# Kernel tuning notes

Hardware: AMD Instinct MI355X
Metric: run time of the kernel (lower is better)

The kernel has to match this reference:

```python
import jax, jax.numpy as jnp
import numpy as np

B, N, D_IN, D_OUT = 16, 2048, 128, 128

def setup_inputs() -> dict:
    key = jax.random.key(0)
    ks = jax.random.split(key, 8)
    x = jax.random.normal(ks[0], (B, N, D_IN), dtype=jnp.float32)
    adj = jax.random.randint(ks[1], (N, N), 0, 2).astype(jnp.float32)
    # Conv1d(kernel_size=1) weights, PyTorch default uniform init scale
    s_emb = 1.0 / np.sqrt(D_IN)
    W_emb = jax.random.uniform(ks[2], (D_OUT, D_IN), jnp.float32, -s_emb, s_emb)
    b_emb = jax.random.uniform(ks[3], (D_OUT,), jnp.float32, -s_emb, s_emb)
    s_qk = 1.0 / np.sqrt(D_OUT)
    w_q = jax.random.uniform(ks[4], (D_OUT,), jnp.float32, -s_qk, s_qk)
    b_q = jax.random.uniform(ks[5], (1,), jnp.float32, -s_qk, s_qk)
    w_k = jax.random.uniform(ks[6], (D_OUT,), jnp.float32, -s_qk, s_qk)
    b_k = jax.random.uniform(ks[7], (1,), jnp.float32, -s_qk, s_qk)
    return {"x": x, "adj": adj, "W_emb": W_emb, "b_emb": b_emb,
            "w_q": w_q, "b_q": b_q, "w_k": w_k, "b_k": b_k}

def reference(x, adj, W_emb, b_emb, w_q, b_q, w_k, b_k):
    # emb_conv: 1x1 conv over node dim == per-node linear  [B,N,D_out]
    seq_fts = jnp.einsum('bni,oi->bno', x, W_emb) + b_emb
    # q_conv / k_conv: project to scalar per node  [B,N]
    q = jnp.einsum('bnd,d->bn', seq_fts, w_q) + b_q  # f_1_t squeezed
    k = jnp.einsum('bnd,d->bn', seq_fts, w_k) + b_k  # f_2_t squeezed
    # f[b,i,j] = f_1_t[b,0,j] + f_2_t^T[b,i,0] = q[b,j] + k[b,i]
    f = k[:, :, None] + q[:, None, :]                 # [B,N,N]
    f = jax.nn.leaky_relu(adj[None, :, :] * f, negative_slope=0.01)
    coefs = jax.nn.softmax(f, axis=1)                 # softmax over dim=1 (rows)
    vals = jnp.einsum('bij,bjd->bid', coefs, seq_fts)  # [B,N,D_out]
    return vals
```

## Files before the change

kernel.cpp:

```cpp
#include <hip/hip_runtime.h>
#include <hip/hip_bf16.h>
#include <stdint.h>

#define B_ 16
#define N_ 2048
#define D_ 128

typedef __bf16 bf16_t;
typedef bf16_t bf16x8 __attribute__((ext_vector_type(8)));
typedef float f32x4 __attribute__((ext_vector_type(4)));

__global__ __launch_bounds__(256) void k_pack_adj(const float* __restrict__ adj,
                                                  unsigned int* __restrict__ bits) {
    int t = blockIdx.x * 256 + threadIdx.x;
    float v = adj[t];
    unsigned long long m = __ballot(v > 0.5f);
    if ((t & 63) == 0) {
        int i = t >> 11;
        int j = t & 2047;
        bits[i * 64 + (j >> 5)]     = (unsigned int)m;
        bits[i * 64 + (j >> 5) + 1] = (unsigned int)(m >> 32);
    }
}

__global__ __launch_bounds__(256, 2) void k_emb(const float* __restrict__ x,
                                                const float* __restrict__ W,
                                                const float* __restrict__ be,
                                                const float* __restrict__ wq,
                                                const float* __restrict__ bq,
                                                const float* __restrict__ wk,
                                                const float* __restrict__ bk,
                                                float* __restrict__ sfT,
                                                float* __restrict__ qa, float* __restrict__ ka,
                                                float* __restrict__ Eq, float* __restrict__ eqs,
                                                float* __restrict__ Ek, float* __restrict__ eks) {
    __shared__ float xs[32][68];
    __shared__ float ws[32][132];
    __shared__ float qs[64], ks[64];
    int b  = blockIdx.y;
    int n0 = blockIdx.x * 64;
    int tid = threadIdx.x;
    int tx = tid & 15, ty = tid >> 4;
    if (tid < 64) { qs[tid] = 0.f; ks[tid] = 0.f; }

    float acc[4][8] = {};
    f32x4 xr[2], wr[4];

    auto loadregs = [&](int kc) {
#pragma unroll
        for (int s = 0; s < 2; ++s) {
            int p = tid + 256 * s;
            int n = p >> 3, kq = p & 7;
            xr[s] = *(const f32x4*)(x + ((size_t)(b * N_ + n0 + n)) * D_ + kc * 32 + kq * 4);
        }
#pragma unroll
        for (int s = 0; s < 4; ++s) {
            int p = tid + 256 * s;
            int d = p >> 3, kq = p & 7;
            wr[s] = *(const f32x4*)(W + (size_t)d * D_ + kc * 32 + kq * 4);
        }
    };
    auto writelds = [&]() {
#pragma unroll
        for (int s = 0; s < 2; ++s) {
            int p = tid + 256 * s;
            int n = p >> 3, kq = p & 7;
#pragma unroll
            for (int u = 0; u < 4; ++u) xs[kq * 4 + u][n] = xr[s][u];
        }
#pragma unroll
        for (int s = 0; s < 4; ++s) {
            int p = tid + 256 * s;
            int d = p >> 3, kq = p & 7;
#pragma unroll
            for (int u = 0; u < 4; ++u) ws[kq * 4 + u][d] = wr[s][u];
        }
    };

    loadregs(0);
    for (int kc = 0; kc < 4; ++kc) {
        writelds();
        __syncthreads();
        if (kc < 3) loadregs(kc + 1);
#pragma unroll 4
        for (int k = 0; k < 32; ++k) {
            f32x4 xv  = *(const f32x4*)&xs[k][tx * 4];
            f32x4 wv0 = *(const f32x4*)&ws[k][ty * 8];
            f32x4 wv1 = *(const f32x4*)&ws[k][ty * 8 + 4];
#pragma unroll
            for (int i = 0; i < 4; ++i)
#pragma unroll
                for (int j = 0; j < 8; ++j)
                    acc[i][j] += xv[i] * ((j < 4) ? wv0[j] : wv1[j - 4]);
        }
        __syncthreads();
    }

    float qp[4] = {}, kp[4] = {};
#pragma unroll
    for (int j = 0; j < 8; ++j) {
        int d = ty * 8 + j;
        float bj  = be[d];
        float wqj = wq[d];
        float wkj = wk[d];
        f32x4 o;
#pragma unroll
        for (int i = 0; i < 4; ++i) {
            o[i] = acc[i][j] + bj;
            qp[i] += o[i] * wqj;
            kp[i] += o[i] * wkj;
        }
        *(f32x4*)(sfT + ((size_t)b * D_ + d) * N_ + n0 + tx * 4) = o;
    }
#pragma unroll
    for (int i = 0; i < 4; ++i) {
        atomicAdd(&qs[tx * 4 + i], qp[i]);
        atomicAdd(&ks[tx * 4 + i], kp[i]);
    }
    __syncthreads();
    if (tid < 64) {
        int idx = b * N_ + n0 + tid;
        float aq = qs[tid] + bq[0];
        float ak = ks[tid] + bk[0];
        qa[idx] = aq;          ka[idx] = ak;
        Eq[idx] = expf(aq);    eqs[idx] = expf(0.01f * aq);
        Ek[idx] = expf(ak);    eks[idx] = expf(0.01f * ak);
    }
}

__global__ __launch_bounds__(256) void k_denom(const unsigned int* __restrict__ bits,
                                               const float* __restrict__ qa,
                                               const float* __restrict__ ka,
                                               const float* __restrict__ Eq,
                                               const float* __restrict__ eqs,
                                               const float* __restrict__ Ek,
                                               const float* __restrict__ eks,
                                               float* __restrict__ denom) {
    int jt  = blockIdx.x;
    int b   = blockIdx.y;
    int seg = blockIdx.z;
    int j = jt * 256 + threadIdx.x;
    float qj  = qa[b * N_ + j];
    float Eqj = Eq[b * N_ + j];
    float eqj = eqs[b * N_ + j];
    int shift = j & 31;
    int wid   = j >> 5;
    float acc = 0.f;
    int i0 = seg * 256;
#pragma unroll 16
    for (int i = i0; i < i0 + 256; ++i) {
        float kk  = ka[b * N_ + i];
        float Ekk = Ek[b * N_ + i];
        float ekk = eks[b * N_ + i];
        unsigned int w = bits[i * 64 + wid];
        float z  = kk + qj;
        float f1 = z > 0.f ? Ekk : ekk;
        float f2 = z > 0.f ? Eqj : eqj;
        float v  = f1 * f2;
        acc += ((w >> shift) & 1u) ? v : 1.0f;
    }
    atomicAdd(&denom[b * N_ + j], acc);
}

__global__ __launch_bounds__(256) void k_scale(const float* __restrict__ sfT,
                                               const float* __restrict__ denom,
                                               bf16_t* __restrict__ Pt) {
    size_t t4 = ((size_t)blockIdx.x * 256 + threadIdx.x) * 4;
    int j  = (int)(t4 & (N_ - 1));
    int b  = (int)(t4 >> 18);
    f32x4 sv = *(const f32x4*)(sfT + t4);
    f32x4 dv = *(const f32x4*)(denom + b * N_ + j);
    bf16_t o[4];
#pragma unroll
    for (int u = 0; u < 4; ++u)
        o[u] = (bf16_t)(sv[u] * __builtin_amdgcn_rcpf(dv[u]));
    *(uint2*)(Pt + t4) = *(uint2*)o;
}

__global__ __launch_bounds__(512, 2) void k_attn(const float* __restrict__ qa,
                                                 const float* __restrict__ ka,
                                                 const float* __restrict__ Eq,
                                                 const float* __restrict__ eqs,
                                                 const float* __restrict__ Ek,
                                                 const float* __restrict__ eks,
                                                 const unsigned int* __restrict__ bits,
                                                 const bf16_t* __restrict__ Pt,
                                                 float* __restrict__ out) {
    __shared__ __align__(16) bf16_t lds[2][128 * 64];
    int b     = blockIdx.y;
    int ibase = blockIdx.x * 128;
    int tid   = threadIdx.x;
    int w     = tid >> 6;
    int lane  = tid & 63;
    int m16   = lane & 15;
    int quad  = lane >> 4;
    int ig    = w & 3;
    int d0    = (w >> 2) * 64;
    int i0    = ibase + ig * 32;

    int iA = i0 + m16, iB = i0 + 16 + m16;
    float kR0  = ka[b * N_ + iA],  kR1  = ka[b * N_ + iB];
    float EkR0 = Ek[b * N_ + iA],  EkR1 = Ek[b * N_ + iB];
    float ekR0 = eks[b * N_ + iA], ekR1 = eks[b * N_ + iB];
    const unsigned int* br0 = bits + (size_t)iA * 64;
    const unsigned int* br1 = bits + (size_t)iB * 64;
    const float* qp  = qa  + b * N_;
    const float* Eqp = Eq  + b * N_;
    const float* eqp = eqs + b * N_;
    const bf16_t* PtB = Pt + (size_t)b * D_ * N_;

    f32x4 acc[2][4];
#pragma unroll
    for (int c = 0; c < 2; ++c)
#pragma unroll
        for (int nt = 0; nt < 4; ++nt) acc[c][nt] = (f32x4){0.f, 0.f, 0.f, 0.f};

    auto stage = [&](int bufi, int jb) {
#pragma unroll
        for (int t = 0; t < 2; ++t) {
            int off = (w * 2 + t) * 1024 + lane * 16;
            int d   = off >> 7;
            int g   = ((off & 127) >> 4) ^ (d & 7);
            const bf16_t* gp = PtB + (size_t)d * N_ + jb + g * 8;
            __builtin_amdgcn_global_load_lds(
                (const __attribute__((address_space(1))) void*)gp,
                (__attribute__((address_space(3))) void*)((char*)(&lds[bufi][0]) + (w * 2 + t) * 1024),
                16, 0, 0);
        }
    };

    stage(0, 0);
    __syncthreads();
    int buf = 0;
    for (int step = 0; step < N_ / 64; ++step) {
        int jb = step * 64;
        if (step + 1 < N_ / 64) stage(buf ^ 1, jb + 64);

        f32x4 q0[2], q1[2], E0[2], E1[2], e0[2], e1[2];
#pragma unroll
        for (int h = 0; h < 2; ++h) {
            int j0 = jb + h * 32 + quad * 8;
            q0[h] = *(const f32x4*)(qp  + j0);
            q1[h] = *(const f32x4*)(qp  + j0 + 4);
            E0[h] = *(const f32x4*)(Eqp + j0);
            E1[h] = *(const f32x4*)(Eqp + j0 + 4);
            e0[h] = *(const f32x4*)(eqp + j0);
            e1[h] = *(const f32x4*)(eqp + j0 + 4);
        }
        uint2 wb0 = *(const uint2*)&br0[jb >> 5];
        uint2 wb1 = *(const uint2*)&br1[jb >> 5];

        bf16x8 af[2][2];
#pragma unroll
        for (int h = 0; h < 2; ++h) {
            unsigned int w0 = h ? wb0.y : wb0.x;
            unsigned int w1 = h ? wb1.y : wb1.x;
#pragma unroll
            for (int t = 0; t < 8; ++t) {
                float qv = (t < 4) ? q0[h][t] : q1[h][t - 4];
                float Ev = (t < 4) ? E0[h][t] : E1[h][t - 4];
                float ev = (t < 4) ? e0[h][t] : e1[h][t - 4];
                int bit = quad * 8 + t;
                {
                    float z = kR0 + qv;
                    float v = ((z > 0.f) ? EkR0 : ekR0) * ((z > 0.f) ? Ev : ev);
                    af[0][h][t] = (bf16_t)(((w0 >> bit) & 1u) ? v : 1.0f);
                }
                {
                    float z = kR1 + qv;
                    float v = ((z > 0.f) ? EkR1 : ekR1) * ((z > 0.f) ? Ev : ev);
                    af[1][h][t] = (bf16_t)(((w1 >> bit) & 1u) ? v : 1.0f);
                }
            }
        }

#pragma unroll
        for (int h = 0; h < 2; ++h) {
            int cph = ((h * 4 + quad) ^ (m16 & 7)) * 8;
#pragma unroll
            for (int nt = 0; nt < 4; ++nt) {
                int d = d0 + nt * 16 + m16;
                bf16x8 bf = *(const bf16x8*)&lds[buf][d * 64 + cph];
                acc[0][nt] = __builtin_amdgcn_mfma_f32_16x16x32_bf16(af[0][h], bf, acc[0][nt], 0, 0, 0);
                acc[1][nt] = __builtin_amdgcn_mfma_f32_16x16x32_bf16(af[1][h], bf, acc[1][nt], 0, 0, 0);
            }
        }
        __syncthreads();
        buf ^= 1;
    }

#pragma unroll
    for (int c = 0; c < 2; ++c) {
        int irow = i0 + c * 16 + quad * 4;
#pragma unroll
        for (int nt = 0; nt < 4; ++nt) {
            int d = d0 + nt * 16 + m16;
#pragma unroll
            for (int r = 0; r < 4; ++r)
                out[((size_t)b * N_ + irow + r) * D_ + d] = acc[c][nt][r];
        }
    }
}

extern "C" void kernel_launch(void* const* d_in, const int* in_sizes, int n_in,
                              void* d_out, int out_size, void* d_ws, size_t ws_size,
                              hipStream_t stream) {
    const float* x   = (const float*)d_in[0];
    const float* adj = (const float*)d_in[1];
    const float* W   = (const float*)d_in[2];
    const float* be  = (const float*)d_in[3];
    const float* wq  = (const float*)d_in[4];
    const float* bq  = (const float*)d_in[5];
    const float* wk  = (const float*)d_in[6];
    const float* bk  = (const float*)d_in[7];
    float* out = (float*)d_out;

    char* ws = (char*)d_ws;
    size_t off = 0;
    float* sfT = (float*)(ws + off);  off += (size_t)B_ * D_ * N_ * 4;
    bf16_t* Pt = (bf16_t*)(ws + off); off += (size_t)B_ * D_ * N_ * 2;
    float* qa  = (float*)(ws + off);  off += (size_t)B_ * N_ * 4;
    float* ka  = (float*)(ws + off);  off += (size_t)B_ * N_ * 4;
    float* denom = (float*)(ws + off); off += (size_t)B_ * N_ * 4;
    float* Eq  = (float*)(ws + off);  off += (size_t)B_ * N_ * 4;
    float* eqs = (float*)(ws + off);  off += (size_t)B_ * N_ * 4;
    float* Ek  = (float*)(ws + off);  off += (size_t)B_ * N_ * 4;
    float* eks = (float*)(ws + off);  off += (size_t)B_ * N_ * 4;
    unsigned int* bits = (unsigned int*)(ws + off); off += (size_t)N_ * 64 * 4;

    hipMemsetAsync(denom, 0, (size_t)B_ * N_ * 4, stream);

    k_pack_adj<<<N_ * N_ / 256, 256, 0, stream>>>(adj, bits);
    k_emb<<<dim3(N_ / 64, B_), 256, 0, stream>>>(x, W, be, wq, bq, wk, bk,
                                                 sfT, qa, ka, Eq, eqs, Ek, eks);
    k_denom<<<dim3(8, 16, 8), 256, 0, stream>>>(bits, qa, ka, Eq, eqs, Ek, eks, denom);
    k_scale<<<B_ * D_ * N_ / 1024, 256, 0, stream>>>(sfT, denom, Pt);
    k_attn<<<dim3(N_ / 128, B_), 512, 0, stream>>>(qa, ka, Eq, eqs, Ek, eks, bits, Pt, out);
}
```

Before: 216.1 us.

## Share computed attention A-fragments across waves via LDS in k_attn

Measured after the change: 204.3 us. -5.5%, faster.

```diff
diff --git a/kernel.cpp b/kernel.cpp
--- a/kernel.cpp
+++ b/kernel.cpp
@@ -177,7 +177,7 @@
     *(uint2*)(Pt + t4) = *(uint2*)o;
 }
 
-__global__ __launch_bounds__(512, 2) void k_attn(const float* __restrict__ qa,
+__global__ __launch_bounds__(256, 2) void k_attn(const float* __restrict__ qa,
                                                  const float* __restrict__ ka,
                                                  const float* __restrict__ Eq,
                                                  const float* __restrict__ eqs,
@@ -186,24 +186,26 @@
                                                  const unsigned int* __restrict__ bits,
                                                  const bf16_t* __restrict__ Pt,
                                                  float* __restrict__ out) {
-    __shared__ __align__(16) bf16_t lds[2][128 * 64];
+    __shared__ __align__(16) bf16_t ldsB[2][128 * 64];
+    __shared__ __align__(16) bf16_t ldsA[4 * 2 * 64 * 8];
     int b     = blockIdx.y;
-    int ibase = blockIdx.x * 128;
+    int ibase = blockIdx.x * 64;
     int tid   = threadIdx.x;
     int w     = tid >> 6;
     int lane  = tid & 63;
     int m16   = lane & 15;
     int quad  = lane >> 4;
-    int ig    = w & 3;
-    int d0    = (w >> 2) * 64;
-    int i0    = ibase + ig * 32;
-
-    int iA = i0 + m16, iB = i0 + 16 + m16;
+    int ig    = w & 1;
+    int dg    = w >> 1;
+    int h     = dg;
+
+    int iA = ibase + (2 * ig) * 16 + m16;
+    int iB = iA + 16;
     float kR0  = ka[b * N_ + iA],  kR1  = ka[b * N_ + iB];
     float EkR0 = Ek[b * N_ + iA],  EkR1 = Ek[b * N_ + iB];
     float ekR0 = eks[b * N_ + iA], ekR1 = eks[b * N_ + iB];
-    const unsigned int* br0 = bits + (size_t)iA * 64;
-    const unsigned int* br1 = bits + (size_t)iB * 64;
+    const unsigned int* brA = bits + (size_t)iA * 64;
+    const unsigned int* brB = bits + (size_t)iB * 64;
     const float* qp  = qa  + b * N_;
     const float* Eqp = Eq  + b * N_;
     const float* eqp = eqs + b * N_;
@@ -217,14 +219,14 @@
 
     auto stage = [&](int bufi, int jb) {
 #pragma unroll
-        for (int t = 0; t < 2; ++t) {
-            int off = (w * 2 + t) * 1024 + lane * 16;
+        for (int t = 0; t < 4; ++t) {
+            int off = t * 4096 + tid * 16;
             int d   = off >> 7;
             int g   = ((off & 127) >> 4) ^ (d & 7);
             const bf16_t* gp = PtB + (size_t)d * N_ + jb + g * 8;
             __builtin_amdgcn_global_load_lds(
                 (const __attribute__((address_space(1))) void*)gp,
-                (__attribute__((address_space(3))) void*)((char*)(&lds[bufi][0]) + (w * 2 + t) * 1024),
+                (__attribute__((address_space(3))) void*)((char*)(&ldsB[bufi][0]) + off),
                 16, 0, 0);
         }
     };
@@ -234,55 +236,54 @@
     int buf = 0;
     for (int step = 0; step < N_ / 64; ++step) {
         int jb = step * 64;
+
+        int j0 = jb + h * 32 + quad * 8;
+        f32x4 q0 = *(const f32x4*)(qp  + j0);
+        f32x4 q1 = *(const f32x4*)(qp  + j0 + 4);
+        f32x4 E0 = *(const f32x4*)(Eqp + j0);
+        f32x4 E1 = *(const f32x4*)(Eqp + j0 + 4);
+        f32x4 e0 = *(const f32x4*)(eqp + j0);
+        f32x4 e1 = *(const f32x4*)(eqp + j0 + 4);
+        unsigned int wA = brA[(jb >> 5) + h];
+        unsigned int wB = brB[(jb >> 5) + h];
+        __builtin_amdgcn_sched_barrier(0);
+
         if (step + 1 < N_ / 64) stage(buf ^ 1, jb + 64);
 
-        f32x4 q0[2], q1[2], E0[2], E1[2], e0[2], e1[2];
-#pragma unroll
-        for (int h = 0; h < 2; ++h) {
-            int j0 = jb + h * 32 + quad * 8;
-            q0[h] = *(const f32x4*)(qp  + j0);
-            q1[h] = *(const f32x4*)(qp  + j0 + 4);
-            E0[h] = *(const f32x4*)(Eqp + j0);
-            E1[h] = *(const f32x4*)(Eqp + j0 + 4);
-            e0[h] = *(const f32x4*)(eqp + j0);
-            e1[h] = *(const f32x4*)(eqp + j0 + 4);
-        }
-        uint2 wb0 = *(const uint2*)&br0[jb >> 5];
-        uint2 wb1 = *(const uint2*)&br1[jb >> 5];
-
-        bf16x8 af[2][2];
-#pragma unroll
-        for (int h = 0; h < 2; ++h) {
-            unsigned int w0 = h ? wb0.y : wb0.x;
-            unsigned int w1 = h ? wb1.y : wb1.x;
-#pragma unroll
-            for (int t = 0; t < 8; ++t) {
-                float qv = (t < 4) ? q0[h][t] : q1[h][t - 4];
-                float Ev = (t < 4) ? E0[h][t] : E1[h][t - 4];
-                float ev = (t < 4) ? e0[h][t] : e1[h][t - 4];
-                int bit = quad * 8 + t;
-                {
-                    float z = kR0 + qv;
-                    float v = ((z > 0.f) ? EkR0 : ekR0) * ((z > 0.f) ? Ev : ev);
-                    af[0][h][t] = (bf16_t)(((w0 >> bit) & 1u) ? v : 1.0f);
-                }
-                {
-                    float z = kR1 + qv;
-                    float v = ((z > 0.f) ? EkR1 : ekR1) * ((z > 0.f) ? Ev : ev);
-                    af[1][h][t] = (bf16_t)(((w1 >> bit) & 1u) ? v : 1.0f);
-                }
+        bf16x8 afA, afB;
+#pragma unroll
+        for (int t = 0; t < 8; ++t) {
+            float qv = (t < 4) ? q0[t] : q1[t - 4];
+            float Ev = (t < 4) ? E0[t] : E1[t - 4];
+            float ev = (t < 4) ? e0[t] : e1[t - 4];
+            int bit = quad * 8 + t;
+            {
+                float z = kR0 + qv;
+                float v = ((z > 0.f) ? EkR0 : ekR0) * ((z > 0.f) ? Ev : ev);
+                afA[t] = (bf16_t)(((wA >> bit) & 1u) ? v : 1.0f);
             }
-        }
-
-#pragma unroll
-        for (int h = 0; h < 2; ++h) {
-            int cph = ((h * 4 + quad) ^ (m16 & 7)) * 8;
+            {
+                float z = kR1 + qv;
+                float v = ((z > 0.f) ? EkR1 : ekR1) * ((z > 0.f) ? Ev : ev);
+                afB[t] = (bf16_t)(((wB >> bit) & 1u) ? v : 1.0f);
+            }
+        }
+        *(bf16x8*)((char*)ldsA + ((((2 * ig + 0) * 2 + h) * 64 + lane) * 16)) = afA;
+        *(bf16x8*)((char*)ldsA + ((((2 * ig + 1) * 2 + h) * 64 + lane) * 16)) = afB;
+
+        asm volatile("s_waitcnt lgkmcnt(0)\n\ts_barrier" ::: "memory");
+
+#pragma unroll
+        for (int hh = 0; hh < 2; ++hh) {
+            bf16x8 a0 = *(const bf16x8*)((char*)ldsA + ((((2 * ig + 0) * 2 + hh) * 64 + lane) * 16));
+            bf16x8 a1 = *(const bf16x8*)((char*)ldsA + ((((2 * ig + 1) * 2 + hh) * 64 + lane) * 16));
+            int cph = ((hh * 4 + quad) ^ (m16 & 7)) * 8;
 #pragma unroll
             for (int nt = 0; nt < 4; ++nt) {
-                int d = d0 + nt * 16 + m16;
-                bf16x8 bf = *(const bf16x8*)&lds[buf][d * 64 + cph];
-                acc[0][nt] = __builtin_amdgcn_mfma_f32_16x16x32_bf16(af[0][h], bf, acc[0][nt], 0, 0, 0);
-                acc[1][nt] = __builtin_amdgcn_mfma_f32_16x16x32_bf16(af[1][h], bf, acc[1][nt], 0, 0, 0);
+                int d = dg * 64 + nt * 16 + m16;
+                bf16x8 bf = *(const bf16x8*)&ldsB[buf][d * 64 + cph];
+                acc[0][nt] = __builtin_amdgcn_mfma_f32_16x16x32_bf16(a0, bf, acc[0][nt], 0, 0, 0);
+                acc[1][nt] = __builtin_amdgcn_mfma_f32_16x16x32_bf16(a1, bf, acc[1][nt], 0, 0, 0);
             }
         }
         __syncthreads();
@@ -291,10 +292,10 @@
 
 #pragma unroll
     for (int c = 0; c < 2; ++c) {
-        int irow = i0 + c * 16 + quad * 4;
+        int irow = ibase + (2 * ig + c) * 16 + quad * 4;
 #pragma unroll
         for (int nt = 0; nt < 4; ++nt) {
-            int d = d0 + nt * 16 + m16;
+            int d = dg * 64 + nt * 16 + m16;
 #pragma unroll
             for (int r = 0; r < 4; ++r)
                 out[((size_t)b * N_ + irow + r) * D_ + d] = acc[c][nt][r];
@@ -335,5 +336,5 @@
                                                  sfT, qa, ka, Eq, eqs, Ek, eks);
     k_denom<<<dim3(8, 16, 8), 256, 0, stream>>>(bits, qa, ka, Eq, eqs, Ek, eks, denom);
     k_scale<<<B_ * D_ * N_ / 1024, 256, 0, stream>>>(sfT, denom, Pt);
-    k_attn<<<dim3(N_ / 128, B_), 512, 0, stream>>>(qa, ka, Eq, eqs, Ek, eks, bits, Pt, out);
-}
+    k_attn<<<dim3(N_ / 64, B_), 256, 0, stream>>>(qa, ka, Eq, eqs, Ek, eks, bits, Pt, out);
+}
```
